# Kernel tuning notes

Measured on AMD Instinct MI355X. Metric: run time of the kernel, lower is better.

## Reference

```python
import jax, jax.numpy as jnp
import numpy as np

EPS = 1e-6

def _sobel_kernels():
    kx = np.array([[1, 0, -1], [2, 0, -2], [1, 0, -1]], dtype=np.float32)
    ky = np.array([[1, 2, 1], [0, 0, 0], [-1, -2, -1]], dtype=np.float32)
    # [out=2, in=1, 3, 3]
    return jnp.asarray(np.stack([kx, ky])[:, None, :, :])

def _edge_mag(img):
    # img: [B, 3, H, W] -> per-channel sobel gradient magnitude [B, 3, H-2, W-2]
    B, C, H, W = img.shape
    x = img.reshape(B * C, 1, H, W)
    g = jax.lax.conv_general_dilated(
        x, _sobel_kernels(), window_strides=(1, 1), padding='VALID',
        dimension_numbers=('NCHW', 'OIHW', 'NCHW'))  # [B*C, 2, H-2, W-2]
    gx, gy = g[:, 0], g[:, 1]
    mag = jnp.sqrt(gx * gx + gy * gy)
    return mag.reshape(B, C, H - 2, W - 2)

def setup_inputs() -> dict:
    key = jax.random.key(0)
    k1, k2 = jax.random.split(key)
    shape = (16, 3, 512, 512)
    source = jax.random.uniform(k1, shape, dtype=jnp.float32)
    target = jax.random.uniform(k2, shape, dtype=jnp.float32)
    return {"source": source, "target": target}

def reference(source, target):
    edge_x = _edge_mag(source)
    edge_y = _edge_mag(target)
    diff = edge_x - edge_y
    error = jnp.sqrt(diff * diff + EPS)
    return jnp.sum(error) / source.shape[0]
```

## Files before the change

### kernel.cpp

```cpp
#include <hip/hip_runtime.h>

#define IMG_W 512
#define IMG_H 512
#define OUT_W 510
#define OUT_H 510
#define NPLANE 48
#define RPW 3
#define WPB 4
#define RPB (RPW * WPB)
#define SPP ((OUT_H + RPB - 1) / RPB)
#define NB (NPLANE * SPP)
#define NXCD 8
#define CPX (NB / NXCD)
#define NWIN (RPW + 2)
#define EPS 1e-6f

template <bool ATOMIC>
__global__ __launch_bounds__(256) void sobel_partial_kernel(
    const float* __restrict__ src, const float* __restrict__ tgt,
    float* __restrict__ partial)
{
    const int tid  = threadIdx.x;
    const int lane = tid & 63;
    const int wv   = tid >> 6;
    const int xb   = lane * 8;

    const int b  = (blockIdx.x % NXCD) * CPX + blockIdx.x / NXCD;
    const int p  = b / SPP;
    const int y0 = (b - p * SPP) * RPB + wv * RPW;

    const float* ps = src + (size_t)p * IMG_W * IMG_H + xb;
    const float* pt = tgt + (size_t)p * IMG_W * IMG_H + xb;

    int ir[NWIN];
    #pragma unroll
    for (int r = 0; r < NWIN; ++r) {
        int t = y0 + r;
        ir[r] = (t > IMG_H - 1) ? IMG_H - 1 : t;
    }

    float vS[NWIN][8], vT[NWIN][8];
    auto loadS = [&](int r) {
        const float* q = ps + (size_t)ir[r] * IMG_W;
        float4 a = *reinterpret_cast<const float4*>(q);
        float4 b4 = *reinterpret_cast<const float4*>(q + 4);
        vS[r][0] = a.x; vS[r][1] = a.y; vS[r][2] = a.z; vS[r][3] = a.w;
        vS[r][4] = b4.x; vS[r][5] = b4.y; vS[r][6] = b4.z; vS[r][7] = b4.w;
    };
    auto loadT = [&](int r) {
        const float* q = pt + (size_t)ir[r] * IMG_W;
        float4 a = *reinterpret_cast<const float4*>(q);
        float4 b4 = *reinterpret_cast<const float4*>(q + 4);
        vT[r][0] = a.x; vT[r][1] = a.y; vT[r][2] = a.z; vT[r][3] = a.w;
        vT[r][4] = b4.x; vT[r][5] = b4.y; vT[r][6] = b4.z; vT[r][7] = b4.w;
    };
    loadS(0); loadS(1); loadS(2);
    loadT(0); loadT(1); loadT(2);
    loadS(3); loadT(3);
    loadS(4); loadT(4);

    float e0S[NWIN], e1S[NWIN], e0T[NWIN], e1T[NWIN];
    auto halo = [&](int r) {
        e0S[r] = __shfl_down(vS[r][0], 1, 64);
        e1S[r] = __shfl_down(vS[r][1], 1, 64);
        e0T[r] = __shfl_down(vT[r][0], 1, 64);
        e1T[r] = __shfl_down(vT[r][1], 1, 64);
    };

    auto VS = [&](int r, int k) -> float {
        return k < 8 ? vS[r][k] : (k == 8 ? e0S[r] : e1S[r]);
    };
    auto VT = [&](int r, int k) -> float {
        return k < 8 ? vT[r][k] : (k == 8 ? e0T[r] : e1T[r]);
    };

    float cm[8];
    #pragma unroll
    for (int j = 0; j < 8; ++j) cm[j] = (xb + j < OUT_W) ? 1.0f : 0.0f;

    float acc = 0.0f;

    #pragma unroll
    for (int i = 0; i < RPW; ++i) {
        if (i == 0) { halo(0); halo(1); halo(2); }
        else        { halo(i + 2); }

        const int a = i, bb = i + 1, c = i + 2;
        float rowsum = 0.0f;

        #pragma unroll
        for (int j = 0; j < 8; ++j) {
            float gxs = fmaf(2.0f, VS(bb, j) - VS(bb, j + 2),
                             (VS(a, j) - VS(a, j + 2)) + (VS(c, j) - VS(c, j + 2)));
            float gys = fmaf(2.0f, VS(a, j + 1), VS(a, j) + VS(a, j + 2))
                      - fmaf(2.0f, VS(c, j + 1), VS(c, j) + VS(c, j + 2));
            float ms  = __builtin_amdgcn_sqrtf(fmaf(gxs, gxs, gys * gys));

            float gxt = fmaf(2.0f, VT(bb, j) - VT(bb, j + 2),
                             (VT(a, j) - VT(a, j + 2)) + (VT(c, j) - VT(c, j + 2)));
            float gyt = fmaf(2.0f, VT(a, j + 1), VT(a, j) + VT(a, j + 2))
                      - fmaf(2.0f, VT(c, j + 1), VT(c, j) + VT(c, j + 2));
            float mt  = __builtin_amdgcn_sqrtf(fmaf(gxt, gxt, gyt * gyt));

            float e = fabsf(ms - mt);
            rowsum = fmaf(e, cm[j], rowsum);
        }

        float rm = (y0 + i < OUT_H) ? 1.0f : 0.0f;
        acc = fmaf(rowsum, rm, acc);
    }

    #pragma unroll
    for (int off = 32; off > 0; off >>= 1)
        acc += __shfl_down(acc, off, 64);

    __shared__ float wsum[WPB];
    if (lane == 0) wsum[wv] = acc;
    __syncthreads();
    if (tid == 0) {
        float tot = wsum[0] + wsum[1] + wsum[2] + wsum[3];
        if (ATOMIC) atomicAdd(partial, tot * (1.0f / 16.0f));
        else        partial[blockIdx.x] = tot;
    }
}

__global__ __launch_bounds__(1024) void reduce_kernel(
    const float* __restrict__ partial, float* __restrict__ out)
{
    float acc = 0.0f;
    for (int i = threadIdx.x; i < NB; i += 1024) acc += partial[i];

    #pragma unroll
    for (int off = 32; off > 0; off >>= 1)
        acc += __shfl_down(acc, off, 64);

    __shared__ float wsum[16];
    const int lane = threadIdx.x & 63;
    const int wid  = threadIdx.x >> 6;
    if (lane == 0) wsum[wid] = acc;
    __syncthreads();
    if (wid == 0) {
        float v = (lane < 16) ? wsum[lane] : 0.0f;
        #pragma unroll
        for (int off = 8; off > 0; off >>= 1)
            v += __shfl_down(v, off, 64);
        if (lane == 0) out[0] = v * (1.0f / 16.0f);
    }
}

extern "C" void kernel_launch(void* const* d_in, const int* in_sizes, int n_in,
                              void* d_out, int out_size, void* d_ws, size_t ws_size,
                              hipStream_t stream) {
    const float* src = (const float*)d_in[0];
    const float* tgt = (const float*)d_in[1];
    float* out = (float*)d_out;

    if (ws_size >= (size_t)NB * sizeof(float)) {
        float* partial = (float*)d_ws;
        sobel_partial_kernel<false><<<dim3(NB), dim3(256), 0, stream>>>(src, tgt, partial);
        reduce_kernel<<<dim3(1), dim3(1024), 0, stream>>>(partial, out);
    } else {
        hipMemsetAsync(out, 0, (size_t)out_size * sizeof(float), stream);
        sobel_partial_kernel<true><<<dim3(NB), dim3(256), 0, stream>>>(src, tgt, out);
    }
}
```

Measured before the change: 24.26 us.

## Split each row across two waves with seam loads, halve rows per block

Each wave now covers half of an image row, four columns per lane, and waves are paired per row group. The block covers 6 rows, so the 510 output rows divide evenly and row clamping and masking are removed. The halo at the split between halves comes from an extra float2 load for lane 63, replacing the shuffle value there. The goal is more blocks and waves with fewer registers per thread, for better occupancy and latency hiding. In exchange, halo rows are loaded more often relative to useful work and there are extra small seam loads.

```diff
diff --git a/kernel.cpp b/kernel.cpp
--- a/kernel.cpp
+++ b/kernel.cpp
@@ -7,8 +7,8 @@
 #define NPLANE 48
 #define RPW 3
 #define WPB 4
-#define RPB (RPW * WPB)
-#define SPP ((OUT_H + RPB - 1) / RPB)
+#define RPB 6
+#define SPP (OUT_H / RPB)
 #define NB (NPLANE * SPP)
 #define NXCD 8
 #define CPX (NB / NXCD)
@@ -23,60 +23,66 @@
     const int tid  = threadIdx.x;
     const int lane = tid & 63;
     const int wv   = tid >> 6;
-    const int xb   = lane * 8;
+    const int half = wv & 1;
+    const int rg   = wv >> 1;
+    const int xb   = half * 256 + lane * 4;
 
     const int b  = (blockIdx.x % NXCD) * CPX + blockIdx.x / NXCD;
     const int p  = b / SPP;
-    const int y0 = (b - p * SPP) * RPB + wv * RPW;
+    const int y0 = (b - p * SPP) * RPB + rg * RPW;
 
-    const float* ps = src + (size_t)p * IMG_W * IMG_H + xb;
-    const float* pt = tgt + (size_t)p * IMG_W * IMG_H + xb;
+    const size_t pb = (size_t)p * IMG_W * IMG_H + (size_t)y0 * IMG_W;
+    const float* ps = src + pb + xb;
+    const float* pt = tgt + pb + xb;
+    const int seamoff = half ? 254 : 256;
+    const float* ss = src + pb + seamoff;
+    const float* st = tgt + pb + seamoff;
 
-    int ir[NWIN];
+    float  vS[NWIN][4], vT[NWIN][4];
+    float2 smS[NWIN], smT[NWIN];
+
+    auto loadS = [&](int r) {
+        float4 a = *reinterpret_cast<const float4*>(ps + (size_t)r * IMG_W);
+        vS[r][0] = a.x; vS[r][1] = a.y; vS[r][2] = a.z; vS[r][3] = a.w;
+    };
+    auto loadT = [&](int r) {
+        float4 a = *reinterpret_cast<const float4*>(pt + (size_t)r * IMG_W);
+        vT[r][0] = a.x; vT[r][1] = a.y; vT[r][2] = a.z; vT[r][3] = a.w;
+    };
+
+    loadS(0); loadS(1); loadS(2);
+    loadT(0); loadT(1); loadT(2);
     #pragma unroll
     for (int r = 0; r < NWIN; ++r) {
-        int t = y0 + r;
-        ir[r] = (t > IMG_H - 1) ? IMG_H - 1 : t;
+        smS[r] = *reinterpret_cast<const float2*>(ss + (size_t)r * IMG_W);
+        smT[r] = *reinterpret_cast<const float2*>(st + (size_t)r * IMG_W);
     }
-
-    float vS[NWIN][8], vT[NWIN][8];
-    auto loadS = [&](int r) {
-        const float* q = ps + (size_t)ir[r] * IMG_W;
-        float4 a = *reinterpret_cast<const float4*>(q);
-        float4 b4 = *reinterpret_cast<const float4*>(q + 4);
-        vS[r][0] = a.x; vS[r][1] = a.y; vS[r][2] = a.z; vS[r][3] = a.w;
-        vS[r][4] = b4.x; vS[r][5] = b4.y; vS[r][6] = b4.z; vS[r][7] = b4.w;
-    };
-    auto loadT = [&](int r) {
-        const float* q = pt + (size_t)ir[r] * IMG_W;
-        float4 a = *reinterpret_cast<const float4*>(q);
-        float4 b4 = *reinterpret_cast<const float4*>(q + 4);
-        vT[r][0] = a.x; vT[r][1] = a.y; vT[r][2] = a.z; vT[r][3] = a.w;
-        vT[r][4] = b4.x; vT[r][5] = b4.y; vT[r][6] = b4.z; vT[r][7] = b4.w;
-    };
-    loadS(0); loadS(1); loadS(2);
-    loadT(0); loadT(1); loadT(2);
     loadS(3); loadT(3);
     loadS(4); loadT(4);
 
+    const bool l63 = (lane == 63);
     float e0S[NWIN], e1S[NWIN], e0T[NWIN], e1T[NWIN];
     auto halo = [&](int r) {
-        e0S[r] = __shfl_down(vS[r][0], 1, 64);
-        e1S[r] = __shfl_down(vS[r][1], 1, 64);
-        e0T[r] = __shfl_down(vT[r][0], 1, 64);
-        e1T[r] = __shfl_down(vT[r][1], 1, 64);
+        float a = __shfl_down(vS[r][0], 1, 64);
+        float b2 = __shfl_down(vS[r][1], 1, 64);
+        float c = __shfl_down(vT[r][0], 1, 64);
+        float d = __shfl_down(vT[r][1], 1, 64);
+        e0S[r] = l63 ? smS[r].x : a;
+        e1S[r] = l63 ? smS[r].y : b2;
+        e0T[r] = l63 ? smT[r].x : c;
+        e1T[r] = l63 ? smT[r].y : d;
     };
 
     auto VS = [&](int r, int k) -> float {
-        return k < 8 ? vS[r][k] : (k == 8 ? e0S[r] : e1S[r]);
+        return k < 4 ? vS[r][k] : (k == 4 ? e0S[r] : e1S[r]);
     };
     auto VT = [&](int r, int k) -> float {
-        return k < 8 ? vT[r][k] : (k == 8 ? e0T[r] : e1T[r]);
+        return k < 4 ? vT[r][k] : (k == 4 ? e0T[r] : e1T[r]);
     };
 
-    float cm[8];
+    float cm[4];
     #pragma unroll
-    for (int j = 0; j < 8; ++j) cm[j] = (xb + j < OUT_W) ? 1.0f : 0.0f;
+    for (int j = 0; j < 4; ++j) cm[j] = (xb + j < OUT_W) ? 1.0f : 0.0f;
 
     float acc = 0.0f;
 
@@ -89,7 +95,7 @@
         float rowsum = 0.0f;
 
         #pragma unroll
-        for (int j = 0; j < 8; ++j) {
+        for (int j = 0; j < 4; ++j) {
             float gxs = fmaf(2.0f, VS(bb, j) - VS(bb, j + 2),
                              (VS(a, j) - VS(a, j + 2)) + (VS(c, j) - VS(c, j + 2)));
             float gys = fmaf(2.0f, VS(a, j + 1), VS(a, j) + VS(a, j + 2))
@@ -106,8 +112,7 @@
             rowsum = fmaf(e, cm[j], rowsum);
         }
 
-        float rm = (y0 + i < OUT_H) ? 1.0f : 0.0f;
-        acc = fmaf(rowsum, rm, acc);
+        acc += rowsum;
     }
 
     #pragma unroll
```

Measured after the change: 22.99 us (median of 2 runs). 1.06x faster.
